# Performance work log

Hardware: AMD Instinct MI355X
Metric: run time of the kernel (lower is better)

The kernel has to match this reference:

```python
import jax, jax.numpy as jnp
import numpy as np
from jax import lax

N, S, H, L, E, V = 10000, 20, 512, 2, 100000, 10000


def setup_inputs() -> dict:
    key = jax.random.key(0)
    ks = jax.random.split(key, 12)
    return {
        "emb": jax.random.normal(ks[0], (V, H), jnp.float32),
        "W_ir": jax.random.normal(ks[1], (L, H, H), jnp.float32) * (2.0 / H) ** 0.5,
        "b_ir": jnp.ones((L, H), jnp.float32),
        "W_iz": jax.random.normal(ks[2], (L, H, H), jnp.float32) * (2.0 / H) ** 0.5,
        "b_iz": jnp.ones((L, H), jnp.float32),
        "lin_w": jax.random.normal(ks[3], (1, H), jnp.float32) * (1.0 / H) ** 0.5,
        "lin_b": jnp.zeros((1,), jnp.float32),
        "skip_w": jax.random.uniform(ks[4], (H, H), jnp.float32),
        "skip_b": jax.random.uniform(ks[5], (H,), jnp.float32),
        "walk_idx": jax.random.randint(ks[6], (N, S), 0, V),
        "edge_label_index": jax.random.randint(ks[7], (2, E), 0, N),
    }


def reference(emb, W_ir, b_ir, W_iz, b_iz, lin_w, lin_b, skip_w, skip_b,
              walk_idx, edge_label_index):
    x = emb[walk_idx]                       # [N, S, H]
    hn = jnp.zeros((x.shape[0], emb.shape[1]), x.dtype)
    for l in range(W_ir.shape[0]):
        # gates depend only on x, precompute all steps: F.linear(x, W) = x @ W.T
        h_all = jnp.einsum('nsh,kh->snk', x, W_ir[l]) + b_ir[l]          # [S, N, H]
        z_all = jax.nn.sigmoid(jnp.einsum('nsh,kh->snk', x, W_iz[l]) + b_iz[l])

        def step(h, tz):
            ht, zt = tz
            return (1.0 - zt) * h + zt * ht, None

        hn, _ = lax.scan(step, hn, (h_all, z_all))
    # note: F.dropout result in original is dead (overwritten); omitted
    score = jax.nn.sigmoid(hn @ lin_w.T + lin_b)        # [N, 1]
    node_feat = score[edge_label_index]                  # [2, E, 1]
    pred = jnp.sum(node_feat[0] * node_feat[1], axis=-1)  # [E] ('dot' decode)
    out2 = hn @ skip_w.T + skip_b                        # [N, H]
    return pred, out2
```

## Files before the change

kernel.cpp:

```cpp
#include <hip/hip_runtime.h>

#define H  512
#define NN 10000
#define SS 20
#define VV 100000
#define EE 100000

typedef __bf16 bf16x8 __attribute__((ext_vector_type(8)));
typedef float  f32x4  __attribute__((ext_vector_type(4)));

__device__ __forceinline__ unsigned short f2bf(float f) {
  unsigned u = __builtin_bit_cast(unsigned, f);
  u += 0x7FFFu + ((u >> 16) & 1u);
  return (unsigned short)(u >> 16);
}
__device__ __forceinline__ float bflo(int x) {
  return __builtin_bit_cast(float, (unsigned)x << 16);
}
__device__ __forceinline__ float bfhi(int x) {
  return __builtin_bit_cast(float, (unsigned)x & 0xFFFF0000u);
}
__device__ __forceinline__ float sigm(float x) { return 1.f / (1.f + __expf(-x)); }

__device__ __forceinline__ unsigned cpk(float lo, float hi) {
  unsigned r;
  asm("v_cvt_pk_bf16_f32 %0, %1, %2" : "=v"(r) : "v"(lo), "v"(hi));
  return r;
}
__device__ __forceinline__ void cvt_store8(unsigned short* dst, float4 a, float4 b) {
  int4 v;
  v.x = (int)cpk(a.x, a.y); v.y = (int)cpk(a.z, a.w);
  v.z = (int)cpk(b.x, b.y); v.w = (int)cpk(b.z, b.w);
  *(int4*)dst = v;
}

__device__ __forceinline__ uint2 cvt8_fp8(float4 a, float4 b) {
  int x = __builtin_amdgcn_cvt_pk_fp8_f32(a.x, a.y, 0, false);
  x = __builtin_amdgcn_cvt_pk_fp8_f32(a.z, a.w, x, true);
  int y = __builtin_amdgcn_cvt_pk_fp8_f32(b.x, b.y, 0, false);
  y = __builtin_amdgcn_cvt_pk_fp8_f32(b.z, b.w, y, true);
  uint2 r; r.x = (unsigned)x; r.y = (unsigned)y; return r;
}

__device__ __forceinline__ void pub_barrier() {
  asm volatile("s_waitcnt lgkmcnt(0)\n\ts_barrier" ::: "memory");
}

__launch_bounds__(256, 3)
__global__ void gru_fused(const float* __restrict__ emb,
                          const float* __restrict__ W_ir,
                          const float* __restrict__ W_iz,
                          const float* __restrict__ b_ir,
                          const float* __restrict__ b_iz,
                          const int* __restrict__ walk,
                          unsigned short* __restrict__ hnb) {
  __shared__ __align__(16) unsigned char As[4][80 * 64];

  const int tid = threadIdx.x;
  const int w = tid >> 6, lane = tid & 63;
  const int r = lane & 15, q = lane >> 4;

  const int hwid = blockIdx.y * 16 + blockIdx.x;
  const int j = hwid >> 3;
  const int cg = j & 15;
  const int sb = (hwid & 7) * 6 + (j >> 4);
  const int c0 = cg * 32;

  const int ly = r & 1;
  const int cch = c0 + 8 * w + (r >> 1);
  long long barr[2][16];
  float bias2[2];
  #pragma unroll
  for (int t = 0; t < 2; ++t) {
    const float* wrow = (t ? W_iz : W_ir) + (long)ly * H * H + (long)cch * H;
    #pragma unroll
    for (int u = 0; u < 16; ++u) {
      const float* s = wrow + u * 32 + q * 8;
      uint2 v = cvt8_fp8(*(const float4*)s, *(const float4*)(s + 4));
      barr[t][u] = __builtin_bit_cast(long long, v);
    }
    bias2[t] = (t ? b_iz : b_ir)[ly * H + cch];
  }

  const int row0 = tid >> 3, g0 = tid & 7;
  const bool has2 = (tid < 128);
  const int L0 = 20 * ((row0 >> 2) & 3) + 4 * (row0 >> 4) + (row0 & 3);
  const int sw0 = row0 * 64 + ((g0 ^ ((row0 >> 1) & 7)) * 8);

  const int ngA = (2500 * sb) / 48;
  const int ngB = (2500 * (sb + 1)) / 48;

  int cur0, cur1, cur2;
  {
    const int* wp = walk + ngA * 80 + L0;
    int v0 = wp[0];  v0 = ((unsigned)v0 < VV) ? v0 : 0;
    int v1 = wp[8];  v1 = ((unsigned)v1 < VV) ? v1 : 0;
    int v2 = has2 ? wp[16] : 0; v2 = ((unsigned)v2 < VV) ? v2 : 0;
    cur0 = v0 * H; cur1 = v1 * H; cur2 = v2 * H;
  }

  float4 pa0, pb0, pa1, pb1, pa2 = {0,0,0,0}, pb2 = {0,0,0,0};

  {
    const float* s0 = emb + cur0 + g0 * 8;
    const float* s1 = emb + cur1 + g0 * 8;
    const float* s2 = emb + cur2 + g0 * 8;
    float4 a0 = *(const float4*)s0, b0 = *(const float4*)(s0 + 4);
    float4 a1 = *(const float4*)s1, b1 = *(const float4*)(s1 + 4);
    float4 a2 = {0,0,0,0}, b2 = {0,0,0,0};
    if (has2) { a2 = *(const float4*)s2; b2 = *(const float4*)(s2 + 4); }
    *(uint2*)(&As[0][0] + sw0)        = cvt8_fp8(a0, b0);
    *(uint2*)(&As[0][0] + sw0 + 2048) = cvt8_fp8(a1, b1);
    if (has2) *(uint2*)(&As[0][0] + sw0 + 4096) = cvt8_fp8(a2, b2);
    pa0 = *(const float4*)(s0 + 64); pb0 = *(const float4*)(s0 + 68);
    pa1 = *(const float4*)(s1 + 64); pb1 = *(const float4*)(s1 + 68);
    if (has2) { pa2 = *(const float4*)(s2 + 64); pb2 = *(const float4*)(s2 + 68); }
  }
  pub_barrier();

  f32x4 acc[5][2];
  const f32x4 fz = {0.f, 0.f, 0.f, 0.f};

  for (int ng = ngA; ng < ngB; ++ng) {
    #pragma unroll
    for (int mt = 0; mt < 5; ++mt)
      #pragma unroll
      for (int t = 0; t < 2; ++t) acc[mt][t] = fz;

    const int ngn = (ng + 1 < ngB) ? ng + 1 : ng;
    int nxt0, nxt1, nxt2;
    {
      const int* wp = walk + ngn * 80 + L0;
      int n0 = wp[0];  n0 = ((unsigned)n0 < VV) ? n0 : 0;
      int n1 = wp[8];  n1 = ((unsigned)n1 < VV) ? n1 : 0;
      int n2 = has2 ? wp[16] : 0; n2 = ((unsigned)n2 < VV) ? n2 : 0;
      nxt0 = n0 * H; nxt1 = n1 * H; nxt2 = n2 * H;
    }

    #pragma unroll
    for (int kc = 0; kc < 8; ++kc) {
      {
        unsigned char* An = &As[(kc + 1) & 3][0];
        *(uint2*)(An + sw0)        = cvt8_fp8(pa0, pb0);
        *(uint2*)(An + sw0 + 2048) = cvt8_fp8(pa1, pb1);
        if (has2) *(uint2*)(An + sw0 + 4096) = cvt8_fp8(pa2, pb2);
      }
      {
        const int cix = kc + 2;
        const int off = (cix & 7) * 64;
        const int u0 = (cix < 8) ? cur0 : nxt0;
        pa0 = *(const float4*)(emb + u0 + off + g0 * 8);
        const int u1 = (cix < 8) ? cur1 : nxt1;
        pa1 = *(const float4*)(emb + u1 + off + g0 * 8);
        if (has2) {
          const int u2 = (cix < 8) ? cur2 : nxt2;
          pa2 = *(const float4*)(emb + u2 + off + g0 * 8);
        }
      }
      const unsigned char* Ab = &As[kc & 3][0];
      #pragma unroll
      for (int ks = 0; ks < 2; ++ks) {
        const int sx = r * 64 + (((ks * 4 + q) ^ (r >> 1)) * 8);
        long long a[5];
        #pragma unroll
        for (int mt = 0; mt < 5; ++mt)
          a[mt] = *(const long long*)(Ab + mt * 1024 + sx);
        #pragma unroll
        for (int mt = 0; mt < 5; ++mt)
          #pragma unroll
          for (int t = 0; t < 2; ++t)
            acc[mt][t] = __builtin_amdgcn_mfma_f32_16x16x32_fp8_fp8(
                a[mt], barr[t][kc * 2 + ks], acc[mt][t], 0, 0, 0);
      }
      {
        const int cix = kc + 2;
        const int off = (cix & 7) * 64 + 4;
        const int u0 = (cix < 8) ? cur0 : nxt0;
        pb0 = *(const float4*)(emb + u0 + off + g0 * 8);
        const int u1 = (cix < 8) ? cur1 : nxt1;
        pb1 = *(const float4*)(emb + u1 + off + g0 * 8);
        if (has2) {
          const int u2 = (cix < 8) ? cur2 : nxt2;
          pb2 = *(const float4*)(emb + u2 + off + g0 * 8);
        }
      }
      pub_barrier();
    }

    {
      float hn1 = 0.f, a2 = 1.f, b2 = 0.f;
      #pragma unroll
      for (int s = 0; s < 20; ++s) {
        const float yh = acc[s >> 2][0][s & 3] + bias2[0];
        const float yz = acc[s >> 2][1][s & 3] + bias2[1];
        const float z = sigm(yz);
        hn1 += z * (yh - hn1);
        a2 *= (1.f - z);
        b2 += z * (yh - b2);
      }
      const float u2 = __shfl_xor(hn1, 1);
      if (ly == 1)
        hnb[(long)(ng * 4 + q) * 1024 + cch] = f2bf(a2 * u2 + b2);
    }
    cur0 = nxt0; cur1 = nxt1; cur2 = nxt2;
  }
}

__global__ void score_kernel(const unsigned short* __restrict__ hnb,
                             const float* __restrict__ lin_w,
                             const float* __restrict__ lin_b,
                             float* __restrict__ R) {
  int tid = threadIdx.x;
  int wv = tid >> 6, lane = tid & 63;
  int node = blockIdx.x * 4 + wv;
  int k = lane * 8;
  int4 hv = *(const int4*)(hnb + (long)node * 1024 + k);
  float4 w0 = *(const float4*)(lin_w + k);
  float4 w1 = *(const float4*)(lin_w + k + 4);
  float s = bflo(hv.x) * w0.x + bfhi(hv.x) * w0.y + bflo(hv.y) * w0.z + bfhi(hv.y) * w0.w
          + bflo(hv.z) * w1.x + bfhi(hv.z) * w1.y + bflo(hv.w) * w1.z + bfhi(hv.w) * w1.w;
  #pragma unroll
  for (int off = 32; off > 0; off >>= 1) s += __shfl_down(s, off);
  if (lane == 0) R[256 + (long)node * 512] = sigm(s + lin_b[0]);
}

__global__ void pred_kernel(const int* __restrict__ eli, const float* __restrict__ R,
                            float* __restrict__ out) {
  int e = blockIdx.x * 256 + threadIdx.x;
  if (e < EE) {
    int a = eli[e];       a = (unsigned)a < NN ? a : 0;
    int b = eli[EE + e];  b = (unsigned)b < NN ? b : 0;
    out[e] = R[256 + (long)a * 512] * R[256 + (long)b * 512];
  }
}

__launch_bounds__(256)
__global__ void out2_kernel(const unsigned short* __restrict__ hnb,
                            const float* __restrict__ skip_w,
                            const float* __restrict__ skip_b,
                            float* __restrict__ out2) {
  __shared__ unsigned short Asl[32][520];
  __shared__ unsigned short Bsl[512][40];
  const int tid = threadIdx.x;
  const int lane = tid & 63, wv = tid >> 6;
  const int r = lane & 15, q = lane >> 4;
  const int m0 = blockIdx.x * 32;

  {
    int arow = tid >> 4;
    int acol = (tid & 15) * 32;
    #pragma unroll
    for (int hh = 0; hh < 2; ++hh) {
      int grow = m0 + hh * 16 + arow;
      unsigned short* dst = &Asl[hh * 16 + arow][acol];
      if (grow < NN) {
        const unsigned short* hr = hnb + (long)grow * 1024 + acol;
        *(int4*)(dst)      = *(const int4*)(hr);
        *(int4*)(dst + 8)  = *(const int4*)(hr + 8);
        *(int4*)(dst + 16) = *(const int4*)(hr + 16);
        *(int4*)(dst + 24) = *(const int4*)(hr + 24);
      } else {
        int4 z = {0, 0, 0, 0};
        *(int4*)(dst) = z; *(int4*)(dst + 8) = z;
        *(int4*)(dst + 16) = z; *(int4*)(dst + 24) = z;
      }
    }
  }

  const f32x4 fzero = {0.f, 0.f, 0.f, 0.f};
  f32x4 acc[2][8];
  #pragma unroll
  for (int rg = 0; rg < 2; ++rg)
    #pragma unroll
    for (int i = 0; i < 8; ++i) acc[rg][i] = fzero;

  const int ksub = (tid & 3) * 8;
  const int jb = tid >> 2;

  for (int k0 = 0; k0 < H; k0 += 32) {
    __syncthreads();
    #pragma unroll
    for (int it = 0; it < 8; ++it) {
      int jj = it * 64 + jb;
      const float* src = skip_w + (long)jj * H + k0 + ksub;
      cvt_store8(&Bsl[jj][ksub], *(const float4*)src, *(const float4*)(src + 4));
    }
    __syncthreads();
    bf16x8 af0 = *(const bf16x8*)&Asl[r][k0 + q * 8];
    bf16x8 af1 = *(const bf16x8*)&Asl[16 + r][k0 + q * 8];
    #pragma unroll
    for (int i = 0; i < 8; ++i) {
      bf16x8 bf = *(const bf16x8*)&Bsl[(wv * 8 + i) * 16 + r][q * 8];
      acc[0][i] = __builtin_amdgcn_mfma_f32_16x16x32_bf16(af0, bf, acc[0][i], 0, 0, 0);
      acc[1][i] = __builtin_amdgcn_mfma_f32_16x16x32_bf16(af1, bf, acc[1][i], 0, 0, 0);
    }
  }
  #pragma unroll
  for (int rg = 0; rg < 2; ++rg)
    #pragma unroll
    for (int i = 0; i < 8; ++i) {
      int col = (wv * 8 + i) * 16 + r;
      float sbv = skip_b[col];
      #pragma unroll
      for (int g = 0; g < 4; ++g) {
        int grow = m0 + rg * 16 + q * 4 + g;
        if (grow < NN) out2[(long)grow * H + col] = acc[rg][i][g] + sbv;
      }
    }
}

extern "C" void kernel_launch(void* const* d_in, const int* in_sizes, int n_in,
                              void* d_out, int out_size, void* d_ws, size_t ws_size,
                              hipStream_t stream) {
  const float* emb    = (const float*)d_in[0];
  const float* W_ir   = (const float*)d_in[1];
  const float* b_ir   = (const float*)d_in[2];
  const float* W_iz   = (const float*)d_in[3];
  const float* b_iz   = (const float*)d_in[4];
  const float* lin_w  = (const float*)d_in[5];
  const float* lin_b  = (const float*)d_in[6];
  const float* skip_w = (const float*)d_in[7];
  const float* skip_b = (const float*)d_in[8];
  const int*   walk   = (const int*)d_in[9];
  const int*   eli    = (const int*)d_in[10];
  float* out = (float*)d_out;
  float* R   = out + EE;
  unsigned short* hnb = (unsigned short*)R;

  dim3 g1(16, 48);
  gru_fused<<<g1, 256, 0, stream>>>(emb, W_ir, W_iz, b_ir, b_iz, walk, hnb);
  score_kernel<<<2500, 256, 0, stream>>>(hnb, lin_w, lin_b, R);
  pred_kernel<<<391, 256, 0, stream>>>(eli, R, out);
  out2_kernel<<<313, 256, 0, stream>>>(hnb, skip_w, skip_b, R);
}
```

Baseline: 654.6 us.

## Deepen gather prefetch pipeline, halve barriers, and shrink grid to 512 blocks

The GRU gather/MFMA loop now prefetches embedding chunks three steps ahead with double-buffered registers instead of two. It writes LDS two stages ahead and issues a barrier only every other k-chunk, which cuts synchronisation. The grid shrinks from 768 to 512 blocks with launch bounds lowered to 2 waves/EU, giving one resident wave of blocks across 256 CUs and more registers per thread. The risks are higher register pressure, load imbalance from fewer blocks, and a correctness hazard if the 4-slot LDS ring with sparser barriers allows a write to overtake a read.

```diff
diff --git a/kernel.cpp b/kernel.cpp
--- a/kernel.cpp
+++ b/kernel.cpp
@@ -46,7 +46,7 @@
   asm volatile("s_waitcnt lgkmcnt(0)\n\ts_barrier" ::: "memory");
 }
 
-__launch_bounds__(256, 3)
+__launch_bounds__(256, 2)
 __global__ void gru_fused(const float* __restrict__ emb,
                           const float* __restrict__ W_ir,
                           const float* __restrict__ W_iz,
@@ -61,9 +61,8 @@
   const int r = lane & 15, q = lane >> 4;
 
   const int hwid = blockIdx.y * 16 + blockIdx.x;
-  const int j = hwid >> 3;
-  const int cg = j & 15;
-  const int sb = (hwid & 7) * 6 + (j >> 4);
+  const int cg = (hwid >> 3) & 15;
+  const int sb = ((hwid & 7) << 2) + (hwid >> 7);
   const int c0 = cg * 32;
 
   const int ly = r & 1;
@@ -87,8 +86,8 @@
   const int L0 = 20 * ((row0 >> 2) & 3) + 4 * (row0 >> 4) + (row0 & 3);
   const int sw0 = row0 * 64 + ((g0 ^ ((row0 >> 1) & 7)) * 8);
 
-  const int ngA = (2500 * sb) / 48;
-  const int ngB = (2500 * (sb + 1)) / 48;
+  const int ngA = (2500 * sb) >> 5;
+  const int ngB = (2500 * (sb + 1)) >> 5;
 
   int cur0, cur1, cur2;
   {
@@ -99,7 +98,8 @@
     cur0 = v0 * H; cur1 = v1 * H; cur2 = v2 * H;
   }
 
-  float4 pa0, pb0, pa1, pb1, pa2 = {0,0,0,0}, pb2 = {0,0,0,0};
+  float4 p0a[2], p0b[2], p1a[2], p1b[2], p2a[2], p2b[2];
+  p2a[0] = p2a[1] = p2b[0] = p2b[1] = (float4){0, 0, 0, 0};
 
   {
     const float* s0 = emb + cur0 + g0 * 8;
@@ -112,11 +112,16 @@
     *(uint2*)(&As[0][0] + sw0)        = cvt8_fp8(a0, b0);
     *(uint2*)(&As[0][0] + sw0 + 2048) = cvt8_fp8(a1, b1);
     if (has2) *(uint2*)(&As[0][0] + sw0 + 4096) = cvt8_fp8(a2, b2);
-    pa0 = *(const float4*)(s0 + 64); pb0 = *(const float4*)(s0 + 68);
-    pa1 = *(const float4*)(s1 + 64); pb1 = *(const float4*)(s1 + 68);
-    if (has2) { pa2 = *(const float4*)(s2 + 64); pb2 = *(const float4*)(s2 + 68); }
-  }
-  pub_barrier();
+    a0 = *(const float4*)(s0 + 64); b0 = *(const float4*)(s0 + 68);
+    a1 = *(const float4*)(s1 + 64); b1 = *(const float4*)(s1 + 68);
+    if (has2) { a2 = *(const float4*)(s2 + 64); b2 = *(const float4*)(s2 + 68); }
+    *(uint2*)(&As[1][0] + sw0)        = cvt8_fp8(a0, b0);
+    *(uint2*)(&As[1][0] + sw0 + 2048) = cvt8_fp8(a1, b1);
+    if (has2) *(uint2*)(&As[1][0] + sw0 + 4096) = cvt8_fp8(a2, b2);
+    p0a[0] = *(const float4*)(s0 + 128); p0b[0] = *(const float4*)(s0 + 132);
+    p1a[0] = *(const float4*)(s1 + 128); p1b[0] = *(const float4*)(s1 + 132);
+    if (has2) { p2a[0] = *(const float4*)(s2 + 128); p2b[0] = *(const float4*)(s2 + 132); }
+  }
 
   f32x4 acc[5][2];
   const f32x4 fz = {0.f, 0.f, 0.f, 0.f};
@@ -139,22 +144,27 @@
 
     #pragma unroll
     for (int kc = 0; kc < 8; ++kc) {
+      if ((kc & 1) == 0) pub_barrier();
+
       {
-        unsigned char* An = &As[(kc + 1) & 3][0];
-        *(uint2*)(An + sw0)        = cvt8_fp8(pa0, pb0);
-        *(uint2*)(An + sw0 + 2048) = cvt8_fp8(pa1, pb1);
-        if (has2) *(uint2*)(An + sw0 + 4096) = cvt8_fp8(pa2, pb2);
+        unsigned char* An = &As[(kc + 2) & 3][0];
+        *(uint2*)(An + sw0)        = cvt8_fp8(p0a[kc & 1], p0b[kc & 1]);
+        *(uint2*)(An + sw0 + 2048) = cvt8_fp8(p1a[kc & 1], p1b[kc & 1]);
+        if (has2) *(uint2*)(An + sw0 + 4096) = cvt8_fp8(p2a[kc & 1], p2b[kc & 1]);
       }
       {
-        const int cix = kc + 2;
+        const int cix = kc + 3;
         const int off = (cix & 7) * 64;
         const int u0 = (cix < 8) ? cur0 : nxt0;
-        pa0 = *(const float4*)(emb + u0 + off + g0 * 8);
         const int u1 = (cix < 8) ? cur1 : nxt1;
-        pa1 = *(const float4*)(emb + u1 + off + g0 * 8);
+        const float* s0 = emb + u0 + off + g0 * 8;
+        p0a[cix & 1] = *(const float4*)s0; p0b[cix & 1] = *(const float4*)(s0 + 4);
+        const float* s1 = emb + u1 + off + g0 * 8;
+        p1a[cix & 1] = *(const float4*)s1; p1b[cix & 1] = *(const float4*)(s1 + 4);
         if (has2) {
           const int u2 = (cix < 8) ? cur2 : nxt2;
-          pa2 = *(const float4*)(emb + u2 + off + g0 * 8);
+          const float* s2 = emb + u2 + off + g0 * 8;
+          p2a[cix & 1] = *(const float4*)s2; p2b[cix & 1] = *(const float4*)(s2 + 4);
         }
       }
       const unsigned char* Ab = &As[kc & 3][0];
@@ -172,19 +182,6 @@
             acc[mt][t] = __builtin_amdgcn_mfma_f32_16x16x32_fp8_fp8(
                 a[mt], barr[t][kc * 2 + ks], acc[mt][t], 0, 0, 0);
       }
-      {
-        const int cix = kc + 2;
-        const int off = (cix & 7) * 64 + 4;
-        const int u0 = (cix < 8) ? cur0 : nxt0;
-        pb0 = *(const float4*)(emb + u0 + off + g0 * 8);
-        const int u1 = (cix < 8) ? cur1 : nxt1;
-        pb1 = *(const float4*)(emb + u1 + off + g0 * 8);
-        if (has2) {
-          const int u2 = (cix < 8) ? cur2 : nxt2;
-          pb2 = *(const float4*)(emb + u2 + off + g0 * 8);
-        }
-      }
-      pub_barrier();
     }
 
     {
@@ -327,7 +324,7 @@
   float* R   = out + EE;
   unsigned short* hnb = (unsigned short*)R;
 
-  dim3 g1(16, 48);
+  dim3 g1(16, 32);
   gru_fused<<<g1, 256, 0, stream>>>(emb, W_ir, W_iz, b_ir, b_iz, walk, hnb);
   score_kernel<<<2500, 256, 0, stream>>>(hnb, lin_w, lin_b, R);
   pred_kernel<<<391, 256, 0, stream>>>(eli, R, out);
```

New measurement: 683.3 us. 1.04x slower.

## Stage embedding gather via global_load_lds DMA into fp32 LDS buffers

Applied to the files above, without the earlier changes.

Replaces register-staged float4 prefetch of embedding rows with direct global-to-LDS loads (global_load_lds, 16 bytes per lane) into a double-buffered fp32 LDS area. Each chunk is then read from LDS, converted to fp8 and written into a double-buffered swizzled A tile. The aim is to free VGPRs and let DMA overlap with MFMA work. In exchange it adds LDS footprint and a vmcnt(0) barrier at the top of every k-chunk, which may expose load latency.

```diff
diff --git a/kernel.cpp b/kernel.cpp
--- a/kernel.cpp
+++ b/kernel.cpp
@@ -42,8 +42,10 @@
   uint2 r; r.x = (unsigned)x; r.y = (unsigned)y; return r;
 }
 
-__device__ __forceinline__ void pub_barrier() {
-  asm volatile("s_waitcnt lgkmcnt(0)\n\ts_barrier" ::: "memory");
+typedef __attribute__((address_space(1))) const unsigned int gu32_t;
+typedef __attribute__((address_space(3))) unsigned int lu32_t;
+__device__ __forceinline__ void dma16(const float* g, float* l) {
+  __builtin_amdgcn_global_load_lds((gu32_t*)g, (lu32_t*)l, 16, 0, 0);
 }
 
 __launch_bounds__(256, 3)
@@ -54,7 +56,8 @@
                           const float* __restrict__ b_iz,
                           const int* __restrict__ walk,
                           unsigned short* __restrict__ hnb) {
-  __shared__ __align__(16) unsigned char As[4][80 * 64];
+  __shared__ __align__(16) float fbuf[2][80 * 64];
+  __shared__ __align__(16) unsigned char As[2][80 * 64];
 
   const int tid = threadIdx.x;
   const int w = tid >> 6, lane = tid & 63;
@@ -82,41 +85,55 @@
     bias2[t] = (t ? b_iz : b_ir)[ly * H + cch];
   }
 
+  const int s4 = lane >> 4;
+  const int c4 = (lane & 15) * 4;
+  int L[5];
+  #pragma unroll
+  for (int jj = 0; jj < 5; ++jj) {
+    const int t5 = w * 5 + jj;
+    L[jj] = 20 * (t5 & 3) + 4 * (t5 >> 2) + s4;
+  }
+  const int dmaw = w * 1280;
+
   const int row0 = tid >> 3, g0 = tid & 7;
   const bool has2 = (tid < 128);
-  const int L0 = 20 * ((row0 >> 2) & 3) + 4 * (row0 >> 4) + (row0 & 3);
   const int sw0 = row0 * 64 + ((g0 ^ ((row0 >> 1) & 7)) * 8);
+  const int fo0 = row0 * 64 + g0 * 8;
 
   const int ngA = (2500 * sb) / 48;
   const int ngB = (2500 * (sb + 1)) / 48;
 
-  int cur0, cur1, cur2;
+  int ncur[5];
   {
-    const int* wp = walk + ngA * 80 + L0;
-    int v0 = wp[0];  v0 = ((unsigned)v0 < VV) ? v0 : 0;
-    int v1 = wp[8];  v1 = ((unsigned)v1 < VV) ? v1 : 0;
-    int v2 = has2 ? wp[16] : 0; v2 = ((unsigned)v2 < VV) ? v2 : 0;
-    cur0 = v0 * H; cur1 = v1 * H; cur2 = v2 * H;
-  }
-
-  float4 pa0, pb0, pa1, pb1, pa2 = {0,0,0,0}, pb2 = {0,0,0,0};
+    const int* wp = walk + ngA * 80;
+    #pragma unroll
+    for (int jj = 0; jj < 5; ++jj) {
+      int v = wp[L[jj]]; v = ((unsigned)v < VV) ? v : 0;
+      ncur[jj] = v * H;
+    }
+  }
 
   {
-    const float* s0 = emb + cur0 + g0 * 8;
-    const float* s1 = emb + cur1 + g0 * 8;
-    const float* s2 = emb + cur2 + g0 * 8;
-    float4 a0 = *(const float4*)s0, b0 = *(const float4*)(s0 + 4);
-    float4 a1 = *(const float4*)s1, b1 = *(const float4*)(s1 + 4);
-    float4 a2 = {0,0,0,0}, b2 = {0,0,0,0};
-    if (has2) { a2 = *(const float4*)s2; b2 = *(const float4*)(s2 + 4); }
-    *(uint2*)(&As[0][0] + sw0)        = cvt8_fp8(a0, b0);
-    *(uint2*)(&As[0][0] + sw0 + 2048) = cvt8_fp8(a1, b1);
-    if (has2) *(uint2*)(&As[0][0] + sw0 + 4096) = cvt8_fp8(a2, b2);
-    pa0 = *(const float4*)(s0 + 64); pb0 = *(const float4*)(s0 + 68);
-    pa1 = *(const float4*)(s1 + 64); pb1 = *(const float4*)(s1 + 68);
-    if (has2) { pa2 = *(const float4*)(s2 + 64); pb2 = *(const float4*)(s2 + 68); }
-  }
-  pub_barrier();
+    float* fb0 = &fbuf[0][0] + dmaw;
+    float* fb1 = &fbuf[1][0] + dmaw;
+    #pragma unroll
+    for (int jj = 0; jj < 5; ++jj)
+      dma16(emb + ncur[jj] + c4, fb0 + jj * 256);
+    #pragma unroll
+    for (int jj = 0; jj < 5; ++jj)
+      dma16(emb + ncur[jj] + 64 + c4, fb1 + jj * 256);
+    asm volatile("s_waitcnt vmcnt(5) lgkmcnt(0)\n\ts_barrier" ::: "memory");
+    const float* fs = &fbuf[0][0];
+    unsigned char* An = &As[0][0];
+    const float* p = fs + fo0;
+    *(uint2*)(An + sw0) = cvt8_fp8(*(const float4*)p, *(const float4*)(p + 4));
+    p += 2048;
+    *(uint2*)(An + sw0 + 2048) = cvt8_fp8(*(const float4*)p, *(const float4*)(p + 4));
+    if (has2) {
+      p += 2048;
+      *(uint2*)(An + sw0 + 4096) = cvt8_fp8(*(const float4*)p, *(const float4*)(p + 4));
+    }
+  }
 
   f32x4 acc[5][2];
   const f32x4 fz = {0.f, 0.f, 0.f, 0.f};
@@ -128,36 +145,45 @@
       for (int t = 0; t < 2; ++t) acc[mt][t] = fz;
 
     const int ngn = (ng + 1 < ngB) ? ng + 1 : ng;
-    int nxt0, nxt1, nxt2;
+    int nnxt[5];
     {
-      const int* wp = walk + ngn * 80 + L0;
-      int n0 = wp[0];  n0 = ((unsigned)n0 < VV) ? n0 : 0;
-      int n1 = wp[8];  n1 = ((unsigned)n1 < VV) ? n1 : 0;
-      int n2 = has2 ? wp[16] : 0; n2 = ((unsigned)n2 < VV) ? n2 : 0;
-      nxt0 = n0 * H; nxt1 = n1 * H; nxt2 = n2 * H;
+      const int* wp = walk + ngn * 80;
+      #pragma unroll
+      for (int jj = 0; jj < 5; ++jj) {
+        int v = wp[L[jj]]; v = ((unsigned)v < VV) ? v : 0;
+        nnxt[jj] = v * H;
+      }
     }
 
     #pragma unroll
     for (int kc = 0; kc < 8; ++kc) {
-      {
-        unsigned char* An = &As[(kc + 1) & 3][0];
-        *(uint2*)(An + sw0)        = cvt8_fp8(pa0, pb0);
-        *(uint2*)(An + sw0 + 2048) = cvt8_fp8(pa1, pb1);
-        if (has2) *(uint2*)(An + sw0 + 4096) = cvt8_fp8(pa2, pb2);
-      }
+      asm volatile("s_waitcnt vmcnt(0) lgkmcnt(0)\n\ts_barrier" ::: "memory");
+
       {
         const int cix = kc + 2;
         const int off = (cix & 7) * 64;
-        const int u0 = (cix < 8) ? cur0 : nxt0;
-        pa0 = *(const float4*)(emb + u0 + off + g0 * 8);
-        const int u1 = (cix < 8) ? cur1 : nxt1;
-        pa1 = *(const float4*)(emb + u1 + off + g0 * 8);
+        float* fb = &fbuf[kc & 1][0] + dmaw;
+        #pragma unroll
+        for (int jj = 0; jj < 5; ++jj) {
+          const int nb = (cix < 8) ? ncur[jj] : nnxt[jj];
+          dma16(emb + nb + off + c4, fb + jj * 256);
+        }
+      }
+
+      {
+        const float* fs = &fbuf[(kc + 1) & 1][0];
+        unsigned char* An = &As[(kc + 1) & 1][0];
+        const float* p = fs + fo0;
+        *(uint2*)(An + sw0) = cvt8_fp8(*(const float4*)p, *(const float4*)(p + 4));
+        p += 2048;
+        *(uint2*)(An + sw0 + 2048) = cvt8_fp8(*(const float4*)p, *(const float4*)(p + 4));
         if (has2) {
-          const int u2 = (cix < 8) ? cur2 : nxt2;
-          pa2 = *(const float4*)(emb + u2 + off + g0 * 8);
+          p += 2048;
+          *(uint2*)(An + sw0 + 4096) = cvt8_fp8(*(const float4*)p, *(const float4*)(p + 4));
         }
       }
-      const unsigned char* Ab = &As[kc & 3][0];
+
+      const unsigned char* Ab = &As[kc & 1][0];
       #pragma unroll
       for (int ks = 0; ks < 2; ++ks) {
         const int sx = r * 64 + (((ks * 4 + q) ^ (r >> 1)) * 8);
@@ -172,19 +198,6 @@
             acc[mt][t] = __builtin_amdgcn_mfma_f32_16x16x32_fp8_fp8(
                 a[mt], barr[t][kc * 2 + ks], acc[mt][t], 0, 0, 0);
       }
-      {
-        const int cix = kc + 2;
-        const int off = (cix & 7) * 64 + 4;
-        const int u0 = (cix < 8) ? cur0 : nxt0;
-        pb0 = *(const float4*)(emb + u0 + off + g0 * 8);
-        const int u1 = (cix < 8) ? cur1 : nxt1;
-        pb1 = *(const float4*)(emb + u1 + off + g0 * 8);
-        if (has2) {
-          const int u2 = (cix < 8) ? cur2 : nxt2;
-          pb2 = *(const float4*)(emb + u2 + off + g0 * 8);
-        }
-      }
-      pub_barrier();
     }
 
     {
@@ -202,7 +215,8 @@
       if (ly == 1)
         hnb[(long)(ng * 4 + q) * 1024 + cch] = f2bf(a2 * u2 + b2);
     }
-    cur0 = nxt0; cur1 = nxt1; cur2 = nxt2;
+    #pragma unroll
+    for (int jj = 0; jj < 5; ++jj) ncur[jj] = nnxt[jj];
   }
 }
 
```

Result: slower. 753.4 us (+15.1%).
